# Optimization experiments

Hardware: AMD Instinct MI355X
Metric: run time of the kernel (lower is better)

## Reference

```python
import jax, jax.numpy as jnp
import numpy as np

B, H, S, DK = 2, 16, 2048, 64
NEG = jnp.float32(-10000.0)


def setup_inputs() -> dict:
    key = jax.random.key(0)
    kq, kk, kv, km = jax.random.split(key, 4)
    query = jax.random.normal(kq, (B, H, S, DK), dtype=jnp.float32)
    k_ = jax.random.normal(kk, (B, H, S, DK), dtype=jnp.float32)
    value = jax.random.normal(kv, (B, H, S, DK), dtype=jnp.float32)
    mask = (jax.random.uniform(km, (B, 1, S, S)) > 0.5).astype(jnp.float32)
    return {"query": query, "key": k_, "value": value, "mask": mask, "d_k": DK}


def reference(query, key, value, mask, d_k):
    # scores: [B,H,S,S]
    scale = jnp.float32(1.0 / np.sqrt(d_k))
    scores = jnp.einsum('bhqd,bhkd->bhqk', query, key) * scale * mask
    # non-standard masking: keep only strictly positive masked scores
    scores = jnp.where(scores > 0, scores, NEG)
    attn = jax.nn.softmax(scores, axis=-1)
    return jnp.einsum('bhqk,bhkd->bhqd', attn, value)
```

## Files before the change

kernel.cpp:

```cpp
#include <hip/hip_runtime.h>
#include <math.h>

#define S_LEN 2048
#define D_KV  64
#define BQ    128
#define BK    64
#define NT    (S_LEN / BK)

typedef __attribute__((ext_vector_type(8))) short bh8;
typedef __attribute__((ext_vector_type(4))) float fx4;
typedef __attribute__((ext_vector_type(4))) unsigned int u32x4;
typedef __attribute__((ext_vector_type(2))) unsigned int u32x2;

__device__ __forceinline__ unsigned cvt2(float a, float b) {
    unsigned r;
    asm("v_cvt_pk_bf16_f32 %0, %1, %2" : "=v"(r) : "v"(a), "v"(b));
    return r;
}

__device__ __forceinline__ int kswz(int row, int byteoff) {
    return ((row << 7) + byteoff) ^ ((row & 7) << 4);
}
__device__ __forceinline__ int vswz(int d, int colb) {
    return ((d << 7) + colb) ^ (((d >> 2) & 7) << 4);
}

__global__ __launch_bounds__(512, 4)
void attn_fwd(const float* __restrict__ Qg, const float* __restrict__ Kg,
              const float* __restrict__ Vg, const float* __restrict__ Mg,
              float* __restrict__ Og)
{
    __shared__ __align__(16) char smem[16384];
    short* kb = (short*)smem;
    short* vb = (short*)(smem + 8192);

    const int tid  = threadIdx.x;
    const int wave = tid >> 6;
    const int lane = tid & 63;
    const int g    = lane >> 4;
    const int c    = lane & 15;

    const int flat = blockIdx.x + (int)gridDim.x * blockIdx.y;
    const int nsw  = (flat & 7) * 64 + (flat >> 3);
    const int qt = nsw & 15;
    const int bh = nsw >> 4;
    const int b  = bh >> 4;

    const int qbase = qt * BQ + wave * 16;

    const float* Kp = Kg + (size_t)bh * S_LEN * D_KV;
    const float* Vp = Vg + (size_t)bh * S_LEN * D_KV;
    const float* Qp = Qg + ((size_t)bh * S_LEN + qbase) * D_KV;
    const float* mrow = Mg + (size_t)b * S_LEN * S_LEN
                      + (size_t)(qbase + c) * S_LEN + g * 4;

    bh8 qf[2];
#pragma unroll
    for (int kc = 0; kc < 2; ++kc) {
        const float* src = Qp + c * D_KV + kc * 32 + g * 8;
        fx4 a0 = *(const fx4*)(src);
        fx4 a1 = *(const fx4*)(src + 4);
        u32x4 q4 = { cvt2(a0[0] * 0.125f, a0[1] * 0.125f),
                     cvt2(a0[2] * 0.125f, a0[3] * 0.125f),
                     cvt2(a1[0] * 0.125f, a1[1] * 0.125f),
                     cvt2(a1[2] * 0.125f, a1[3] * 0.125f) };
        qf[kc] = __builtin_bit_cast(bh8, q4);
    }

    const bool isK = (tid < 256);
    const int  stid = tid & 255;
    const int  vk0 = (stid >> 4) << 2;
    const int  vd0 = (stid & 15) << 2;
    const int  vcolb = (((vk0 & 15) >> 2) << 5) + ((vk0 >> 4) << 3);

    fx4 kvr[4];

    auto issue_kv = [&](int kt) {
        if (isK) {
#pragma unroll
            for (int i = 0; i < 4; ++i) {
                const int idx = stid + 256 * i;
                kvr[i] = *(const fx4*)(Kp + (size_t)(kt + (idx >> 4)) * D_KV
                                          + ((idx & 15) << 2));
            }
        } else {
            const float* vsrc = Vp + (size_t)(kt + vk0) * D_KV + vd0;
#pragma unroll
            for (int i = 0; i < 4; ++i)
                kvr[i] = *(const fx4*)(vsrc + i * D_KV);
        }
    };
    auto write_kv = [&]() {
        if (isK) {
#pragma unroll
            for (int i = 0; i < 4; ++i) {
                const int idx = stid + 256 * i;
                const int kr  = idx >> 4;
                const int de  = (idx & 15) << 2;
                u32x2 w = { cvt2(kvr[i][0], kvr[i][1]), cvt2(kvr[i][2], kvr[i][3]) };
                *(u32x2*)((char*)kb + kswz(kr, de << 1)) = w;
            }
        } else {
#pragma unroll
            for (int i = 0; i < 4; ++i) {
                u32x2 w = { cvt2(kvr[0][i], kvr[1][i]), cvt2(kvr[2][i], kvr[3][i]) };
                *(u32x2*)((char*)vb + vswz(vd0 + i, vcolb)) = w;
            }
        }
    };

    fx4 o[4];
#pragma unroll
    for (int u = 0; u < 4; ++u) { fx4 z = {0.f, 0.f, 0.f, 0.f}; o[u] = z; }
    float l = 0.f;

    issue_kv(0);

#pragma unroll 1
    for (int t = 0; t < NT; ++t) {
        const int kt = t * BK;

        fx4 mv[4];
#pragma unroll
        for (int tt = 0; tt < 4; ++tt)
            mv[tt] = *(const fx4*)(mrow + kt + tt * 16);

        write_kv();
        __syncthreads();

        if (t + 1 < NT) issue_kv(kt + BK);

        fx4 st[4];
#pragma unroll
        for (int tt = 0; tt < 4; ++tt) { fx4 z = {0.f, 0.f, 0.f, 0.f}; st[tt] = z; }
        __builtin_amdgcn_s_setprio(1);
#pragma unroll
        for (int kc = 0; kc < 2; ++kc) {
#pragma unroll
            for (int tt = 0; tt < 4; ++tt) {
                bh8 kf = *(const bh8*)((char*)kb + kswz(tt * 16 + c, (kc << 6) + (g << 4)));
                st[tt] = __builtin_amdgcn_mfma_f32_16x16x32_bf16(kf, qf[kc], st[tt], 0, 0, 0);
            }
        }
        __builtin_amdgcn_s_setprio(0);

        unsigned pk[8];
#pragma unroll
        for (int tt = 0; tt < 4; ++tt) {
            float tm0 = st[tt][0] * mv[tt][0];
            float tm1 = st[tt][1] * mv[tt][1];
            float tm2 = st[tt][2] * mv[tt][2];
            float tm3 = st[tt][3] * mv[tt][3];
            float p0 = tm0 > 0.f ? __expf(tm0) : 0.f;
            float p1 = tm1 > 0.f ? __expf(tm1) : 0.f;
            float p2 = tm2 > 0.f ? __expf(tm2) : 0.f;
            float p3 = tm3 > 0.f ? __expf(tm3) : 0.f;
            l += (p0 + p1) + (p2 + p3);
            pk[tt * 2 + 0] = cvt2(p0, p1);
            pk[tt * 2 + 1] = cvt2(p2, p3);
        }

        __builtin_amdgcn_s_setprio(1);
#pragma unroll
        for (int tp = 0; tp < 2; ++tp) {
            u32x4 pq = { pk[tp * 4 + 0], pk[tp * 4 + 1],
                         pk[tp * 4 + 2], pk[tp * 4 + 3] };
            bh8 pp = __builtin_bit_cast(bh8, pq);
#pragma unroll
            for (int u = 0; u < 4; ++u) {
                bh8 vv = *(const bh8*)((char*)vb + vswz(u * 16 + c, (g << 5) + (tp << 4)));
                o[u] = __builtin_amdgcn_mfma_f32_16x16x32_bf16(vv, pp, o[u], 0, 0, 0);
            }
        }
        __builtin_amdgcn_s_setprio(0);

        __syncthreads();
    }

    l += __shfl_xor(l, 16);
    l += __shfl_xor(l, 32);
    const float inv = 1.0f / l;

    float* orow = Og + ((size_t)bh * S_LEN + qbase + c) * D_KV + g * 4;
#pragma unroll
    for (int u = 0; u < 4; ++u) {
        fx4 r = o[u] * inv;
        *(fx4*)(orow + u * 16) = r;
    }
}

extern "C" void kernel_launch(void* const* d_in, const int* in_sizes, int n_in,
                              void* d_out, int out_size, void* d_ws, size_t ws_size,
                              hipStream_t stream) {
    const float* Q = (const float*)d_in[0];
    const float* K = (const float*)d_in[1];
    const float* V = (const float*)d_in[2];
    const float* M = (const float*)d_in[3];
    float*       O = (float*)d_out;
    dim3 grid(S_LEN / BQ, 32);
    attn_fwd<<<grid, 512, 0, stream>>>(Q, K, V, M, O);
}
```

Measured before the change: 198.8 us.

## Switch attention to 32x32x16 MFMA with 4 waves of 32 query rows

Replaces the 16x16x32 bf16 MFMA tiling with 32x32x16 MFMA. Each of 4 waves (256 threads) now owns 32 query rows instead of 16 per wave across 8 waves. P fragments are rearranged with v_permlane32_swap for the PV product. Softmax and PV are split into two halves so exp work on one half can overlap MFMA on the other, and the mask loads are split accordingly. This aims for higher MFMA efficiency and fewer LDS reads per FLOP, at the cost of fewer waves per block and more registers per thread.

```diff
diff --git a/kernel.cpp b/kernel.cpp
--- a/kernel.cpp
+++ b/kernel.cpp
@@ -7,25 +7,25 @@
 #define BK    64
 #define NT    (S_LEN / BK)
 
-typedef __attribute__((ext_vector_type(8))) short bh8;
-typedef __attribute__((ext_vector_type(4))) float fx4;
-typedef __attribute__((ext_vector_type(4))) unsigned int u32x4;
-typedef __attribute__((ext_vector_type(2))) unsigned int u32x2;
+typedef __attribute__((ext_vector_type(8)))  short bh8;
+typedef __attribute__((ext_vector_type(4)))  float fx4;
+typedef __attribute__((ext_vector_type(16))) float fx16;
+typedef __attribute__((ext_vector_type(4)))  unsigned int u32x4;
+typedef __attribute__((ext_vector_type(2)))  unsigned int u32x2;
 
 __device__ __forceinline__ unsigned cvt2(float a, float b) {
     unsigned r;
     asm("v_cvt_pk_bf16_f32 %0, %1, %2" : "=v"(r) : "v"(a), "v"(b));
     return r;
 }
-
-__device__ __forceinline__ int kswz(int row, int byteoff) {
-    return ((row << 7) + byteoff) ^ ((row & 7) << 4);
-}
-__device__ __forceinline__ int vswz(int d, int colb) {
-    return ((d << 7) + colb) ^ (((d >> 2) & 7) << 4);
-}
-
-__global__ __launch_bounds__(512, 4)
+__device__ __forceinline__ void swap32(unsigned &d, unsigned &s) {
+    asm("v_permlane32_swap_b32 %0, %1" : "+v"(d), "+v"(s));
+}
+__device__ __forceinline__ int swz(int row, int byteoff) {
+    return (row << 7) + (byteoff ^ ((row & 7) << 4));
+}
+
+__global__ __launch_bounds__(256, 3)
 void attn_fwd(const float* __restrict__ Qg, const float* __restrict__ Kg,
               const float* __restrict__ Vg, const float* __restrict__ Mg,
               float* __restrict__ Og)
@@ -35,10 +35,10 @@
     short* vb = (short*)(smem + 8192);
 
     const int tid  = threadIdx.x;
+    const int lane = tid & 63;
     const int wave = tid >> 6;
-    const int lane = tid & 63;
-    const int g    = lane >> 4;
-    const int c    = lane & 15;
+    const int lq   = lane & 31;
+    const int hf   = lane >> 5;
 
     const int flat = blockIdx.x + (int)gridDim.x * blockIdx.y;
     const int nsw  = (flat & 7) * 64 + (flat >> 3);
@@ -46,146 +46,167 @@
     const int bh = nsw >> 4;
     const int b  = bh >> 4;
 
-    const int qbase = qt * BQ + wave * 16;
+    const int qbase = qt * BQ + wave * 32;
 
     const float* Kp = Kg + (size_t)bh * S_LEN * D_KV;
     const float* Vp = Vg + (size_t)bh * S_LEN * D_KV;
     const float* Qp = Qg + ((size_t)bh * S_LEN + qbase) * D_KV;
     const float* mrow = Mg + (size_t)b * S_LEN * S_LEN
-                      + (size_t)(qbase + c) * S_LEN + g * 4;
-
-    bh8 qf[2];
-#pragma unroll
-    for (int kc = 0; kc < 2; ++kc) {
-        const float* src = Qp + c * D_KV + kc * 32 + g * 8;
-        fx4 a0 = *(const fx4*)(src);
+                      + (size_t)(qbase + lq) * S_LEN + hf * 4;
+
+    bh8 qf[4];
+#pragma unroll
+    for (int ks = 0; ks < 4; ++ks) {
+        const float* src = Qp + lq * D_KV + ks * 16 + hf * 8;
+        fx4 a0 = *(const fx4*)src;
         fx4 a1 = *(const fx4*)(src + 4);
         u32x4 q4 = { cvt2(a0[0] * 0.125f, a0[1] * 0.125f),
                      cvt2(a0[2] * 0.125f, a0[3] * 0.125f),
                      cvt2(a1[0] * 0.125f, a1[1] * 0.125f),
                      cvt2(a1[2] * 0.125f, a1[3] * 0.125f) };
-        qf[kc] = __builtin_bit_cast(bh8, q4);
+        qf[ks] = __builtin_bit_cast(bh8, q4);
     }
 
-    const bool isK = (tid < 256);
-    const int  stid = tid & 255;
-    const int  vk0 = (stid >> 4) << 2;
-    const int  vd0 = (stid & 15) << 2;
-    const int  vcolb = (((vk0 & 15) >> 2) << 5) + ((vk0 >> 4) << 3);
-
-    fx4 kvr[4];
-
-    auto issue_kv = [&](int kt) {
-        if (isK) {
-#pragma unroll
-            for (int i = 0; i < 4; ++i) {
-                const int idx = stid + 256 * i;
-                kvr[i] = *(const fx4*)(Kp + (size_t)(kt + (idx >> 4)) * D_KV
-                                          + ((idx & 15) << 2));
-            }
-        } else {
-            const float* vsrc = Vp + (size_t)(kt + vk0) * D_KV + vd0;
-#pragma unroll
-            for (int i = 0; i < 4; ++i)
-                kvr[i] = *(const fx4*)(vsrc + i * D_KV);
-        }
-    };
-    auto write_kv = [&]() {
-        if (isK) {
-#pragma unroll
-            for (int i = 0; i < 4; ++i) {
-                const int idx = stid + 256 * i;
-                const int kr  = idx >> 4;
-                const int de  = (idx & 15) << 2;
-                u32x2 w = { cvt2(kvr[i][0], kvr[i][1]), cvt2(kvr[i][2], kvr[i][3]) };
-                *(u32x2*)((char*)kb + kswz(kr, de << 1)) = w;
-            }
-        } else {
-#pragma unroll
-            for (int i = 0; i < 4; ++i) {
-                u32x2 w = { cvt2(kvr[0][i], kvr[1][i]), cvt2(kvr[2][i], kvr[3][i]) };
-                *(u32x2*)((char*)vb + vswz(vd0 + i, vcolb)) = w;
-            }
-        }
-    };
-
-    fx4 o[4];
-#pragma unroll
-    for (int u = 0; u < 4; ++u) { fx4 z = {0.f, 0.f, 0.f, 0.f}; o[u] = z; }
-    float l = 0.f;
-
-    issue_kv(0);
+    const int krow = tid >> 2;
+    const int kcol = (tid & 3) << 2;
+    const int vd0  = (tid >> 4) << 2;
+    const int vk0  = (tid & 15) << 2;
+
+    fx16 o0 = {}, o1 = {};
+    float lsum = 0.f;
+    fx4 kreg[4], vreg[4];
+
+#pragma unroll
+    for (int i = 0; i < 4; ++i)
+        kreg[i] = *(const fx4*)(Kp + (size_t)krow * D_KV + kcol + 16 * i);
+#pragma unroll
+    for (int i = 0; i < 4; ++i)
+        vreg[i] = *(const fx4*)(Vp + (size_t)(vk0 + i) * D_KV + vd0);
 
 #pragma unroll 1
     for (int t = 0; t < NT; ++t) {
         const int kt = t * BK;
 
-        fx4 mv[4];
-#pragma unroll
-        for (int tt = 0; tt < 4; ++tt)
-            mv[tt] = *(const fx4*)(mrow + kt + tt * 16);
-
-        write_kv();
+        fx4 mv0[4];
+#pragma unroll
+        for (int m = 0; m < 4; ++m)
+            mv0[m] = *(const fx4*)(mrow + kt + m * 8);
+
+#pragma unroll
+        for (int i = 0; i < 4; ++i) {
+            u32x2 w = { cvt2(kreg[i][0], kreg[i][1]),
+                        cvt2(kreg[i][2], kreg[i][3]) };
+            *(u32x2*)((char*)kb + swz(krow, (kcol << 1) + 32 * i)) = w;
+        }
+#pragma unroll
+        for (int i = 0; i < 4; ++i) {
+            u32x2 w = { cvt2(vreg[0][i], vreg[1][i]),
+                        cvt2(vreg[2][i], vreg[3][i]) };
+            *(u32x2*)((char*)vb + swz(vd0 + i, vk0 << 1)) = w;
+        }
         __syncthreads();
 
-        if (t + 1 < NT) issue_kv(kt + BK);
-
-        fx4 st[4];
-#pragma unroll
-        for (int tt = 0; tt < 4; ++tt) { fx4 z = {0.f, 0.f, 0.f, 0.f}; st[tt] = z; }
+        if (t + 1 < NT) {
+            const int kn = kt + BK;
+#pragma unroll
+            for (int i = 0; i < 4; ++i)
+                kreg[i] = *(const fx4*)(Kp + (size_t)(kn + krow) * D_KV + kcol + 16 * i);
+#pragma unroll
+            for (int i = 0; i < 4; ++i)
+                vreg[i] = *(const fx4*)(Vp + (size_t)(kn + vk0 + i) * D_KV + vd0);
+        }
+
+        fx16 st0 = {}, st1 = {};
         __builtin_amdgcn_s_setprio(1);
 #pragma unroll
-        for (int kc = 0; kc < 2; ++kc) {
-#pragma unroll
-            for (int tt = 0; tt < 4; ++tt) {
-                bh8 kf = *(const bh8*)((char*)kb + kswz(tt * 16 + c, (kc << 6) + (g << 4)));
-                st[tt] = __builtin_amdgcn_mfma_f32_16x16x32_bf16(kf, qf[kc], st[tt], 0, 0, 0);
-            }
+        for (int ks = 0; ks < 4; ++ks) {
+            bh8 k0 = *(const bh8*)((char*)kb + swz(lq,      ks * 32 + hf * 16));
+            bh8 k1 = *(const bh8*)((char*)kb + swz(32 + lq, ks * 32 + hf * 16));
+            st0 = __builtin_amdgcn_mfma_f32_32x32x16_bf16(k0, qf[ks], st0, 0, 0, 0);
+            st1 = __builtin_amdgcn_mfma_f32_32x32x16_bf16(k1, qf[ks], st1, 0, 0, 0);
         }
         __builtin_amdgcn_s_setprio(0);
 
-        unsigned pk[8];
-#pragma unroll
-        for (int tt = 0; tt < 4; ++tt) {
-            float tm0 = st[tt][0] * mv[tt][0];
-            float tm1 = st[tt][1] * mv[tt][1];
-            float tm2 = st[tt][2] * mv[tt][2];
-            float tm3 = st[tt][3] * mv[tt][3];
+        fx4 mv1[4];
+#pragma unroll
+        for (int m = 0; m < 4; ++m)
+            mv1[m] = *(const fx4*)(mrow + kt + 32 + m * 8);
+
+        unsigned pkw[16];
+
+#pragma unroll
+        for (int m = 0; m < 4; ++m) {
+            float tm0 = st0[4*m+0] * mv0[m][0];
+            float tm1 = st0[4*m+1] * mv0[m][1];
+            float tm2 = st0[4*m+2] * mv0[m][2];
+            float tm3 = st0[4*m+3] * mv0[m][3];
             float p0 = tm0 > 0.f ? __expf(tm0) : 0.f;
             float p1 = tm1 > 0.f ? __expf(tm1) : 0.f;
             float p2 = tm2 > 0.f ? __expf(tm2) : 0.f;
             float p3 = tm3 > 0.f ? __expf(tm3) : 0.f;
-            l += (p0 + p1) + (p2 + p3);
-            pk[tt * 2 + 0] = cvt2(p0, p1);
-            pk[tt * 2 + 1] = cvt2(p2, p3);
+            lsum += (p0 + p1) + (p2 + p3);
+            pkw[m*2+0] = cvt2(p0, p1);
+            pkw[m*2+1] = cvt2(p2, p3);
         }
 
         __builtin_amdgcn_s_setprio(1);
 #pragma unroll
-        for (int tp = 0; tp < 2; ++tp) {
-            u32x4 pq = { pk[tp * 4 + 0], pk[tp * 4 + 1],
-                         pk[tp * 4 + 2], pk[tp * 4 + 3] };
-            bh8 pp = __builtin_bit_cast(bh8, pq);
-#pragma unroll
-            for (int u = 0; u < 4; ++u) {
-                bh8 vv = *(const bh8*)((char*)vb + vswz(u * 16 + c, (g << 5) + (tp << 4)));
-                o[u] = __builtin_amdgcn_mfma_f32_16x16x32_bf16(vv, pp, o[u], 0, 0, 0);
-            }
+        for (int vp = 0; vp < 2; ++vp) {
+            unsigned w0 = pkw[vp*4+0], w1 = pkw[vp*4+1];
+            unsigned w2 = pkw[vp*4+2], w3 = pkw[vp*4+3];
+            swap32(w0, w2); swap32(w1, w3);
+            u32x4 pq = { w0, w1, w2, w3 };
+            bh8 pb = __builtin_bit_cast(bh8, pq);
+            bh8 v0 = *(const bh8*)((char*)vb + swz(lq,      vp * 32 + hf * 16));
+            bh8 v1 = *(const bh8*)((char*)vb + swz(32 + lq, vp * 32 + hf * 16));
+            o0 = __builtin_amdgcn_mfma_f32_32x32x16_bf16(v0, pb, o0, 0, 0, 0);
+            o1 = __builtin_amdgcn_mfma_f32_32x32x16_bf16(v1, pb, o1, 0, 0, 0);
+        }
+        __builtin_amdgcn_s_setprio(0);
+
+#pragma unroll
+        for (int m = 0; m < 4; ++m) {
+            float tm0 = st1[4*m+0] * mv1[m][0];
+            float tm1 = st1[4*m+1] * mv1[m][1];
+            float tm2 = st1[4*m+2] * mv1[m][2];
+            float tm3 = st1[4*m+3] * mv1[m][3];
+            float p0 = tm0 > 0.f ? __expf(tm0) : 0.f;
+            float p1 = tm1 > 0.f ? __expf(tm1) : 0.f;
+            float p2 = tm2 > 0.f ? __expf(tm2) : 0.f;
+            float p3 = tm3 > 0.f ? __expf(tm3) : 0.f;
+            lsum += (p0 + p1) + (p2 + p3);
+            pkw[8 + m*2+0] = cvt2(p0, p1);
+            pkw[8 + m*2+1] = cvt2(p2, p3);
+        }
+
+        __builtin_amdgcn_s_setprio(1);
+#pragma unroll
+        for (int vp = 2; vp < 4; ++vp) {
+            unsigned w0 = pkw[vp*4+0], w1 = pkw[vp*4+1];
+            unsigned w2 = pkw[vp*4+2], w3 = pkw[vp*4+3];
+            swap32(w0, w2); swap32(w1, w3);
+            u32x4 pq = { w0, w1, w2, w3 };
+            bh8 pb = __builtin_bit_cast(bh8, pq);
+            bh8 v0 = *(const bh8*)((char*)vb + swz(lq,      vp * 32 + hf * 16));
+            bh8 v1 = *(const bh8*)((char*)vb + swz(32 + lq, vp * 32 + hf * 16));
+            o0 = __builtin_amdgcn_mfma_f32_32x32x16_bf16(v0, pb, o0, 0, 0, 0);
+            o1 = __builtin_amdgcn_mfma_f32_32x32x16_bf16(v1, pb, o1, 0, 0, 0);
         }
         __builtin_amdgcn_s_setprio(0);
 
         __syncthreads();
     }
 
-    l += __shfl_xor(l, 16);
-    l += __shfl_xor(l, 32);
-    const float inv = 1.0f / l;
-
-    float* orow = Og + ((size_t)bh * S_LEN + qbase + c) * D_KV + g * 4;
-#pragma unroll
-    for (int u = 0; u < 4; ++u) {
-        fx4 r = o[u] * inv;
-        *(fx4*)(orow + u * 16) = r;
+    lsum += __shfl_xor(lsum, 32);
+    const float inv = 1.0f / lsum;
+
+    float* orow = Og + ((size_t)bh * S_LEN + qbase + lq) * D_KV;
+#pragma unroll
+    for (int m = 0; m < 4; ++m) {
+        fx4 r0 = { o0[4*m+0]*inv, o0[4*m+1]*inv, o0[4*m+2]*inv, o0[4*m+3]*inv };
+        *(fx4*)(orow + m * 8 + hf * 4) = r0;
+        fx4 r1 = { o1[4*m+0]*inv, o1[4*m+1]*inv, o1[4*m+2]*inv, o1[4*m+3]*inv };
+        *(fx4*)(orow + 32 + m * 8 + hf * 4) = r1;
     }
 }
 
@@ -198,5 +219,5 @@
     const float* M = (const float*)d_in[3];
     float*       O = (float*)d_out;
     dim3 grid(S_LEN / BQ, 32);
-    attn_fwd<<<grid, 512, 0, stream>>>(Q, K, V, M, O);
-}
+    attn_fwd<<<grid, 256, 0, stream>>>(Q, K, V, M, O);
+}
```

Measured after the change: 234.8 us. 18.1% more time.
